# Performance work log

Measured on AMD Instinct MI355X. Metric: run time of the kernel, lower is better.

Reference implementation:

```python
import jax, jax.numpy as jnp
import numpy as np

INPUT_DIM = 512
OUTPUT_DIM = 512
DEGREE = 8
BATCH = 16384


def setup_inputs() -> dict:
    key = jax.random.key(0)
    kx, kc = jax.random.split(key)
    x = jax.random.normal(kx, (BATCH, INPUT_DIM), dtype=jnp.float32)
    cheby_coeffs = jax.random.normal(kc, (INPUT_DIM, OUTPUT_DIM, DEGREE + 1), dtype=jnp.float32) / jnp.sqrt(
        jnp.float32(INPUT_DIM * (DEGREE + 1))
    )
    return {"x": x, "cheby_coeffs": cheby_coeffs}


def reference(x, cheby_coeffs):
    degree = cheby_coeffs.shape[-1] - 1
    arange = jnp.arange(degree + 1, dtype=x.dtype)  # [d]
    t = jnp.tanh(x)  # [b, i], squash into [-1, 1]
    theta = jnp.arccos(t)[..., None] * arange  # [b, i, d]
    basis = jnp.cos(theta)  # Chebyshev T_n(tanh(x)) = cos(n * arccos(tanh(x)))
    y = jnp.einsum('bid,iod->bo', basis, cheby_coeffs)
    return y
```

## Files before the change

### kernel.cpp

```cpp
#include <hip/hip_runtime.h>
#include <hip/hip_bf16.h>
#include <stdint.h>


#define BM 128
#define BN 128
#define BK 64
#define NSTEPS 64
#define IN_DIM 512
#define OUT_DIM 512

typedef __attribute__((ext_vector_type(8))) short short8;
typedef __attribute__((ext_vector_type(8))) unsigned short ushort8;
typedef __attribute__((ext_vector_type(4))) float f32x4;

__device__ __forceinline__ unsigned short f2bf(float f) {
  __hip_bfloat16 h = __float2bfloat16(f);
  return __builtin_bit_cast(unsigned short, h);
}

__device__ __forceinline__ float fast_tanh(float v) {
  float e = __expf(v + v);
  return 1.0f - 2.0f * __builtin_amdgcn_rcpf(e + 1.0f);
}

__device__ __forceinline__ void gload_lds16(const void* g, void* l) {
  __builtin_amdgcn_global_load_lds(
      (const __attribute__((address_space(1))) unsigned int*)(uintptr_t)g,
      (__attribute__((address_space(3))) unsigned int*)(uintptr_t)l,
      16, 0, 0);
}

__global__ __launch_bounds__(256) void cheby_reorder_b(
    const float* __restrict__ coeffs, unsigned char* __restrict__ bws) {
  const int g = blockIdx.x * 256 + threadIdx.x;
  const int i = g & 511;
  const int o = g >> 9;
  const int nb = o >> 7, nl = o & 127;
  const int itile = i >> 5, il = i & 31;
  const float* cp = coeffs + (size_t)i * 4608 + (size_t)o * 9;
  const int swz = (nl & 7) << 4;
#pragma unroll
  for (int p = 0; p < 4; ++p) {
    const size_t base =
        ((size_t)(nb * 64 + itile * 4 + p) << 14) + (size_t)nl * 128;
    *(unsigned short*)(bws + base + ((il * 2) ^ swz)) = f2bf(cp[1 + 2 * p]);
    *(unsigned short*)(bws + base + ((64 + il * 2) ^ swz)) =
        f2bf(cp[2 + 2 * p]);
  }
}

__global__ __launch_bounds__(64) void cheby_colsum(
    const float* __restrict__ coeffs, float* __restrict__ cs) {
  const int o = blockIdx.x;
  const int l = threadIdx.x;
  float s = 0.0f;
#pragma unroll
  for (int j = 0; j < 8; ++j)
    s += coeffs[(size_t)(l + j * 64) * 4608 + (size_t)o * 9];
#pragma unroll
  for (int off = 32; off > 0; off >>= 1) s += __shfl_down(s, off, 64);
  if (l == 0) cs[o] = s;
}

__global__ __launch_bounds__(256, 3) void cheby_gemm(
    const float* __restrict__ x, const unsigned char* __restrict__ bws,
    const float* __restrict__ colsum, float* __restrict__ out) {
  const int bid = blockIdx.x;
  const int m0 = (bid >> 2) * BM;
  const int nblk = bid & 3;
  const int n0 = nblk * BN;
  const int tid = threadIdx.x;
  const int lane = tid & 63;
  const int wid = tid >> 6;
  const int wm = (wid >> 1) * 64;
  const int wn = (wid & 1) * 64;
  const int l15 = lane & 15;
  const int lhi = lane >> 4;

  __shared__ __align__(16) unsigned char As[BM * 128];
  __shared__ __align__(16) unsigned char Bs[2][BN * 128];

  const int srow = tid >> 1;
  const int ihalf = tid & 1;
  unsigned char* Arow = As + srow * 128;
  const int aswz = (srow & 7) << 4;
  const int wbase = ihalf * 32;

  float t2[16], Tm1[16], Tm2[16];
  f32x4 acc[4][4];
#pragma unroll
  for (int a = 0; a < 4; ++a)
#pragma unroll
    for (int b = 0; b < 4; ++b) acc[a][b] = (f32x4){0.f, 0.f, 0.f, 0.f};

  const unsigned char* bchunk0 = bws + ((size_t)(nblk * 64) << 14);
  const int goff = wid * 4096 + lane * 16;

  {
    const unsigned char* gsrc = bchunk0 + goff;
    unsigned char* ldst = &Bs[0][0] + wid * 4096;
    gload_lds16(gsrc, ldst);
    gload_lds16(gsrc + 1024, ldst + 1024);
    gload_lds16(gsrc + 2048, ldst + 2048);
    gload_lds16(gsrc + 3072, ldst + 3072);
  }

  for (int s = 0; s < NSTEPS; ++s) {
    const int p = s & 1;

    {
      const int snext = (s < NSTEPS - 1) ? s + 1 : NSTEPS - 1;
      const unsigned char* gsrc = bchunk0 + ((size_t)snext << 14) + goff;
      unsigned char* ldst = &Bs[p ^ 1][0] + wid * 4096;
      gload_lds16(gsrc, ldst);
      gload_lds16(gsrc + 1024, ldst + 1024);
      gload_lds16(gsrc + 2048, ldst + 2048);
      gload_lds16(gsrc + 3072, ldst + 3072);
    }

    const int q = s & 3;
    if (q == 0) {
      const int itile = s >> 2;
      const float* xp =
          x + (size_t)(m0 + srow) * IN_DIM + itile * 32 + ihalf * 16;
#pragma unroll
      for (int j = 0; j < 4; ++j) {
        const float4 v = reinterpret_cast<const float4*>(xp)[j];
        const float a0 = fast_tanh(v.x);
        const float a1 = fast_tanh(v.y);
        const float a2 = fast_tanh(v.z);
        const float a3 = fast_tanh(v.w);
        Tm2[4 * j + 0] = a0; Tm2[4 * j + 1] = a1;
        Tm2[4 * j + 2] = a2; Tm2[4 * j + 3] = a3;
        t2[4 * j + 0] = a0 + a0; t2[4 * j + 1] = a1 + a1;
        t2[4 * j + 2] = a2 + a2; t2[4 * j + 3] = a3 + a3;
        Tm1[4 * j + 0] = __builtin_fmaf(a0 + a0, a0, -1.0f);
        Tm1[4 * j + 1] = __builtin_fmaf(a1 + a1, a1, -1.0f);
        Tm1[4 * j + 2] = __builtin_fmaf(a2 + a2, a2, -1.0f);
        Tm1[4 * j + 3] = __builtin_fmaf(a3 + a3, a3, -1.0f);
      }
    } else {
#pragma unroll
      for (int e = 0; e < 16; ++e) {
        const float Ta = __builtin_fmaf(t2[e], Tm1[e], -Tm2[e]);
        const float Tb = __builtin_fmaf(t2[e], Ta, -Tm1[e]);
        Tm2[e] = Ta;
        Tm1[e] = Tb;
      }
    }
    ushort8 pa0, pa1, pb0, pb1;
#pragma unroll
    for (int j = 0; j < 8; ++j) {
      pa0[j] = f2bf(Tm2[j]);
      pa1[j] = f2bf(Tm2[j + 8]);
      pb0[j] = f2bf(Tm1[j]);
      pb1[j] = f2bf(Tm1[j + 8]);
    }
    *(ushort8*)(Arow + ((wbase) ^ aswz)) = pa0;
    *(ushort8*)(Arow + ((wbase + 16) ^ aswz)) = pa1;
    *(ushort8*)(Arow + ((64 + wbase) ^ aswz)) = pb0;
    *(ushort8*)(Arow + ((64 + wbase + 16) ^ aswz)) = pb1;

    asm volatile("s_waitcnt vmcnt(4) lgkmcnt(0)" ::: "memory");
    __builtin_amdgcn_s_barrier();

    const unsigned char* Bcur = &Bs[p][0];
#pragma unroll
    for (int ks = 0; ks < 2; ++ks) {
      short8 af[4];
#pragma unroll
      for (int fm = 0; fm < 4; ++fm) {
        const int row = wm + fm * 16 + l15;
        af[fm] = *(const short8*)(
            As + row * 128 + ((ks * 64 + lhi * 16) ^ ((row & 7) << 4)));
      }
#pragma unroll
      for (int fn = 0; fn < 4; ++fn) {
        const int row = wn + fn * 16 + l15;
        const short8 bf = *(const short8*)(
            Bcur + row * 128 + ((ks * 64 + lhi * 16) ^ ((row & 7) << 4)));
#pragma unroll
        for (int fm = 0; fm < 4; ++fm)
          acc[fm][fn] = __builtin_amdgcn_mfma_f32_16x16x32_bf16(
              af[fm], bf, acc[fm][fn], 0, 0, 0);
      }
    }

    __builtin_amdgcn_s_barrier();
  }

  float csv[4];
#pragma unroll
  for (int fn = 0; fn < 4; ++fn) csv[fn] = colsum[n0 + wn + fn * 16 + l15];
#pragma unroll
  for (int fm = 0; fm < 4; ++fm) {
    const int r0 = m0 + wm + fm * 16 + lhi * 4;
#pragma unroll
    for (int fn = 0; fn < 4; ++fn) {
      const int col = n0 + wn + fn * 16 + l15;
#pragma unroll
      for (int r = 0; r < 4; ++r)
        out[(size_t)(r0 + r) * OUT_DIM + col] = acc[fm][fn][r] + csv[fn];
    }
  }
}

extern "C" void kernel_launch(void* const* d_in, const int* in_sizes, int n_in,
                              void* d_out, int out_size, void* d_ws,
                              size_t ws_size, hipStream_t stream) {
  const float* x = (const float*)d_in[0];
  const float* coeffs = (const float*)d_in[1];
  float* out = (float*)d_out;
  unsigned char* bws = (unsigned char*)d_ws;
  float* cs = (float*)((unsigned char*)d_ws + ((size_t)4 << 20));

  hipLaunchKernelGGL(cheby_reorder_b, dim3(1024), dim3(256), 0, stream, coeffs,
                     bws);
  hipLaunchKernelGGL(cheby_colsum, dim3(512), dim3(64), 0, stream, coeffs, cs);
  hipLaunchKernelGGL(cheby_gemm, dim3(512), dim3(256), 0, stream, x, bws, cs,
                     out);
}
```

Before: 100.7 us.

## Build Chebyshev A-fragments in registers instead of staging through LDS

Each wave now loads its own x rows and computes the tanh/Chebyshev recurrence directly into the MFMA A-operand register layout, removing the shared A tile, its LDS writes, reads and the lgkmcnt wait. Because wave pairs share rows, tanh and the recurrence are computed twice as often overall. The x loads are hoisted ahead of the B prefetch. Register pressure rises (32 values × 3 arrays plus accumulators), so the occupancy hint drops from 3 to 2 blocks.

Result: slower. 113.2 us (+12.5%).

```diff
diff --git a/kernel.cpp b/kernel.cpp
--- a/kernel.cpp
+++ b/kernel.cpp
@@ -5,13 +5,11 @@
 
 #define BM 128
 #define BN 128
-#define BK 64
 #define NSTEPS 64
 #define IN_DIM 512
 #define OUT_DIM 512
 
 typedef __attribute__((ext_vector_type(8))) short short8;
-typedef __attribute__((ext_vector_type(8))) unsigned short ushort8;
 typedef __attribute__((ext_vector_type(4))) float f32x4;
 
 __device__ __forceinline__ unsigned short f2bf(float f) {
@@ -63,7 +61,7 @@
   if (l == 0) cs[o] = s;
 }
 
-__global__ __launch_bounds__(256, 3) void cheby_gemm(
+__global__ __launch_bounds__(256, 2) void cheby_gemm(
     const float* __restrict__ x, const unsigned char* __restrict__ bws,
     const float* __restrict__ colsum, float* __restrict__ out) {
   const int bid = blockIdx.x;
@@ -78,16 +76,14 @@
   const int l15 = lane & 15;
   const int lhi = lane >> 4;
 
-  __shared__ __align__(16) unsigned char As[BM * 128];
   __shared__ __align__(16) unsigned char Bs[2][BN * 128];
 
-  const int srow = tid >> 1;
-  const int ihalf = tid & 1;
-  unsigned char* Arow = As + srow * 128;
-  const int aswz = (srow & 7) << 4;
-  const int wbase = ihalf * 32;
-
-  float t2[16], Tm1[16], Tm2[16];
+  const float* xrow[4];
+#pragma unroll
+  for (int fm = 0; fm < 4; ++fm)
+    xrow[fm] = x + (size_t)(m0 + wm + fm * 16 + l15) * IN_DIM + lhi * 8;
+
+  float t2[4][8], Tm1[4][8], Tm2[4][8];
   f32x4 acc[4][4];
 #pragma unroll
   for (int a = 0; a < 4; ++a)
@@ -108,6 +104,19 @@
 
   for (int s = 0; s < NSTEPS; ++s) {
     const int p = s & 1;
+    const int q = s & 3;
+
+    float4 xa[4], xb[4];
+    if (q == 0) {
+      const int it = s >> 2;
+#pragma unroll
+      for (int fm = 0; fm < 4; ++fm) {
+        const float* xp = xrow[fm] + it * 32;
+        xa[fm] = reinterpret_cast<const float4*>(xp)[0];
+        xb[fm] = reinterpret_cast<const float4*>(xp)[1];
+      }
+      __builtin_amdgcn_sched_barrier(0);
+    }
 
     {
       const int snext = (s < NSTEPS - 1) ? s + 1 : NSTEPS - 1;
@@ -119,83 +128,75 @@
       gload_lds16(gsrc + 3072, ldst + 3072);
     }
 
-    const int q = s & 3;
     if (q == 0) {
-      const int itile = s >> 2;
-      const float* xp =
-          x + (size_t)(m0 + srow) * IN_DIM + itile * 32 + ihalf * 16;
-#pragma unroll
-      for (int j = 0; j < 4; ++j) {
-        const float4 v = reinterpret_cast<const float4*>(xp)[j];
-        const float a0 = fast_tanh(v.x);
-        const float a1 = fast_tanh(v.y);
-        const float a2 = fast_tanh(v.z);
-        const float a3 = fast_tanh(v.w);
-        Tm2[4 * j + 0] = a0; Tm2[4 * j + 1] = a1;
-        Tm2[4 * j + 2] = a2; Tm2[4 * j + 3] = a3;
-        t2[4 * j + 0] = a0 + a0; t2[4 * j + 1] = a1 + a1;
-        t2[4 * j + 2] = a2 + a2; t2[4 * j + 3] = a3 + a3;
-        Tm1[4 * j + 0] = __builtin_fmaf(a0 + a0, a0, -1.0f);
-        Tm1[4 * j + 1] = __builtin_fmaf(a1 + a1, a1, -1.0f);
-        Tm1[4 * j + 2] = __builtin_fmaf(a2 + a2, a2, -1.0f);
-        Tm1[4 * j + 3] = __builtin_fmaf(a3 + a3, a3, -1.0f);
+#pragma unroll
+      for (int fm = 0; fm < 4; ++fm) {
+#pragma unroll
+        for (int j = 0; j < 8; ++j) {
+          const float xv = (j < 4) ? ((const float*)&xa[fm])[j & 3]
+                                   : ((const float*)&xb[fm])[j & 3];
+          const float th = fast_tanh(xv);
+          const float tt = th + th;
+          t2[fm][j] = tt;
+          Tm2[fm][j] = th;
+          Tm1[fm][j] = __builtin_fmaf(tt, th, -1.0f);
+        }
       }
     } else {
 #pragma unroll
-      for (int e = 0; e < 16; ++e) {
-        const float Ta = __builtin_fmaf(t2[e], Tm1[e], -Tm2[e]);
-        const float Tb = __builtin_fmaf(t2[e], Ta, -Tm1[e]);
-        Tm2[e] = Ta;
-        Tm1[e] = Tb;
-      }
-    }
-    ushort8 pa0, pa1, pb0, pb1;
-#pragma unroll
-    for (int j = 0; j < 8; ++j) {
-      pa0[j] = f2bf(Tm2[j]);
-      pa1[j] = f2bf(Tm2[j + 8]);
-      pb0[j] = f2bf(Tm1[j]);
-      pb1[j] = f2bf(Tm1[j + 8]);
-    }
-    *(ushort8*)(Arow + ((wbase) ^ aswz)) = pa0;
-    *(ushort8*)(Arow + ((wbase + 16) ^ aswz)) = pa1;
-    *(ushort8*)(Arow + ((64 + wbase) ^ aswz)) = pb0;
-    *(ushort8*)(Arow + ((64 + wbase + 16) ^ aswz)) = pb1;
-
-    asm volatile("s_waitcnt vmcnt(4) lgkmcnt(0)" ::: "memory");
+      for (int fm = 0; fm < 4; ++fm) {
+#pragma unroll
+        for (int j = 0; j < 8; ++j) {
+          const float Ta = __builtin_fmaf(t2[fm][j], Tm1[fm][j], -Tm2[fm][j]);
+          const float Tb = __builtin_fmaf(t2[fm][j], Ta, -Tm1[fm][j]);
+          Tm2[fm][j] = Ta;
+          Tm1[fm][j] = Tb;
+        }
+      }
+    }
+    short8 af0[4], af1[4];
+#pragma unroll
+    for (int fm = 0; fm < 4; ++fm)
+#pragma unroll
+      for (int j = 0; j < 8; ++j) {
+        af0[fm][j] = (short)f2bf(Tm2[fm][j]);
+        af1[fm][j] = (short)f2bf(Tm1[fm][j]);
+      }
+
+    asm volatile("s_waitcnt vmcnt(4)" ::: "memory");
     __builtin_amdgcn_s_barrier();
 
     const unsigned char* Bcur = &Bs[p][0];
 #pragma unroll
-    for (int ks = 0; ks < 2; ++ks) {
-      short8 af[4];
-#pragma unroll
-      for (int fm = 0; fm < 4; ++fm) {
-        const int row = wm + fm * 16 + l15;
-        af[fm] = *(const short8*)(
-            As + row * 128 + ((ks * 64 + lhi * 16) ^ ((row & 7) << 4)));
-      }
-#pragma unroll
-      for (int fn = 0; fn < 4; ++fn) {
-        const int row = wn + fn * 16 + l15;
-        const short8 bf = *(const short8*)(
-            Bcur + row * 128 + ((ks * 64 + lhi * 16) ^ ((row & 7) << 4)));
-#pragma unroll
-        for (int fm = 0; fm < 4; ++fm)
-          acc[fm][fn] = __builtin_amdgcn_mfma_f32_16x16x32_bf16(
-              af[fm], bf, acc[fm][fn], 0, 0, 0);
-      }
+    for (int fn = 0; fn < 4; ++fn) {
+      const int row = wn + fn * 16 + l15;
+      const int rsw = (row & 7) << 4;
+      const short8 bf0 = *(const short8*)(
+          Bcur + row * 128 + ((lhi * 16) ^ rsw));
+      const short8 bf1 = *(const short8*)(
+          Bcur + row * 128 + ((64 + lhi * 16) ^ rsw));
+#pragma unroll
+      for (int fm = 0; fm < 4; ++fm)
+        acc[fm][fn] = __builtin_amdgcn_mfma_f32_16x16x32_bf16(
+            af0[fm], bf0, acc[fm][fn], 0, 0, 0);
+#pragma unroll
+      for (int fm = 0; fm < 4; ++fm)
+        acc[fm][fn] = __builtin_amdgcn_mfma_f32_16x16x32_bf16(
+            af1[fm], bf1, acc[fm][fn], 0, 0, 0);
     }
 
     __builtin_amdgcn_s_barrier();
   }
 
+  asm volatile("s_waitcnt vmcnt(0)" ::: "memory");
+
   float csv[4];
 #pragma unroll
   for (int fn = 0; fn < 4; ++fn) csv[fn] = colsum[n0 + wn + fn * 16 + l15];
+  const int lhi4 = lhi * 4;
 #pragma unroll
   for (int fm = 0; fm < 4; ++fm) {
-    const int r0 = m0 + wm + fm * 16 + lhi * 4;
+    const int r0 = m0 + wm + fm * 16 + lhi4;
 #pragma unroll
     for (int fn = 0; fn < 4; ++fn) {
       const int col = n0 + wn + fn * 16 + l15;
```
